# Optimization experiments

Measured on AMD Instinct MI355X. Metric: run time of the kernel, lower is better.

Reference implementation:

```python
import jax, jax.numpy as jnp
import numpy as np
import math

B, N, DIM = 8, 8192, 256
DIM_ATTN, HEAD, RANK = 256, 4, 64
HEAD_DIM = DIM_ATTN // HEAD


def setup_inputs() -> dict:
    key = jax.random.key(0)
    ks = jax.random.split(key, 8)
    x = jax.random.normal(ks[0], (B, N, DIM), dtype=jnp.float32)
    z = jax.random.normal(ks[1], (B, N, DIM), dtype=jnp.float32)
    # nn.Linear(dim, dim_attn): weight (out,in) -> use (in,out) for x @ W
    Wq = jax.random.normal(ks[2], (DIM, DIM_ATTN), dtype=jnp.float32) / np.sqrt(DIM)
    bq = jnp.zeros((DIM_ATTN,), dtype=jnp.float32)
    K = jax.random.normal(ks[3], (RANK, HEAD, HEAD_DIM), dtype=jnp.float32)
    Wv = jax.random.normal(ks[4], (DIM, DIM), dtype=jnp.float32) / np.sqrt(DIM)
    bv = jnp.zeros((DIM,), dtype=jnp.float32)
    alpha = jnp.full((HEAD, 1), math.log(9.0), dtype=jnp.float32)
    beta = jnp.full((HEAD, 1), math.log(0.01), dtype=jnp.float32)
    return {"x": x, "z": z, "Wq": Wq, "bq": bq, "K": K, "Wv": Wv, "bv": bv,
            "alpha": alpha, "beta": beta}


def reference(x, z, Wq, bq, K, Wv, bv, alpha, beta):
    b, n, f = x.shape
    # q: (b, n, head, head_dim)
    q = (z @ Wq + bq).reshape(b, n, HEAD, HEAD_DIM)
    # attn scores over latent rank: (b, n, h, r)
    attn = jnp.einsum('bnhd,rhd->bnhr', q, K) / np.sqrt(HEAD_DIM).astype(np.float32)
    # value projection: (b, n, h, d)
    xv = (x @ Wv + bv).reshape(b, n, HEAD, HEAD_DIM)
    # pool over n with softmax over r: (b, r, h, d)
    pooled = jnp.einsum('bnhr,bnhd->brhd', jax.nn.softmax(attn, axis=-1), xv)
    # redistribute with softmax over n: (b, n, h, d)
    v = jnp.einsum('bnhr,brhd->bnhd', jax.nn.softmax(attn, axis=1), pooled)
    # sigmoid-gated combine; alpha/beta are (head, 1) broadcasting over (h, d)
    out = jax.nn.sigmoid(alpha) * xv + jax.nn.sigmoid(beta) * v
    return out.reshape(b, n, f)
```

## Files before the change

### kernel.cpp

```cpp
#include <hip/hip_runtime.h>
#include <hip/hip_bf16.h>

typedef __hip_bfloat16 bf16;
typedef __attribute__((ext_vector_type(8))) __bf16 bf16x8;
typedef __attribute__((ext_vector_type(4))) float f32x4;

#define BB 8
#define NN 8192
#define DIM 256
#define HEAD 4
#define HD 64
#define RANK 64
#define BN (BB*NN)

__device__ __forceinline__ float b2f(bf16 v){ return __bfloat162float(v); }
__device__ __forceinline__ bf16 f2b(float v){ return __float2bfloat16(v); }
__device__ __forceinline__ unsigned short f2bu(float f){
    bf16 h = __float2bfloat16(f);
    return *(unsigned short*)&h;
}
__device__ __forceinline__ float u2f(unsigned short u){
    unsigned int x = ((unsigned int)u) << 16; return __uint_as_float(x);
}
__device__ __forceinline__ __bf16 f2bb(float f){
    bf16 h = __float2bfloat16(f);
    return *reinterpret_cast<__bf16*>(&h);
}
__device__ __forceinline__ int swz(int k, int outer){
    return (((k >> 3) ^ (outer & 7)) << 3) | (k & 7);
}

__global__ void __launch_bounds__(256) kW(
    const float* __restrict__ Wq, const float* __restrict__ bq,
    const float* __restrict__ Km, const float* __restrict__ Wv,
    unsigned short* __restrict__ WattnT, unsigned short* __restrict__ WvT,
    float* __restrict__ battn)
{
    const int c = blockIdx.x;
    const int h = c >> 6, r = c & 63;
    const int t = threadIdx.x;
    __shared__ float Ks[64];
    if(t < 64) Ks[t] = Km[((size_t)r*HEAD + h)*64 + t];
    __syncthreads();

    const float* wqrow = Wq + (size_t)t*DIM + h*64;
    float a = 0.f;
    #pragma unroll
    for(int d = 0; d < 64; d++) a = fmaf(wqrow[d], Ks[d], a);
    WattnT[(size_t)c*DIM + t] = f2bu(0.125f * a);
    WvT[(size_t)c*DIM + t]    = f2bu(Wv[(size_t)t*DIM + c]);
    if(t == 0){
        float bb = 0.f;
        for(int d = 0; d < 64; d++) bb += bq[h*64+d]*Ks[d];
        battn[c] = 0.125f * bb;
    }
}

__global__ void __launch_bounds__(256) kG(
    const float* __restrict__ x, const float* __restrict__ z,
    const unsigned short* __restrict__ WvT, const unsigned short* __restrict__ WattnT,
    const float* __restrict__ bv, const float* __restrict__ battn,
    float* __restrict__ outF, unsigned short* __restrict__ outB,
    float* __restrict__ Pm, float* __restrict__ Ps)
{
    __shared__ __attribute__((aligned(16))) __bf16 As[2][64][40];

    const int role = blockIdx.x & 1;
    const int tile = blockIdx.x >> 1;

    const float* A            = role ? z : x;
    const unsigned short* WT  = role ? WattnT : WvT;
    const float* bias         = role ? battn : bv;

    const int t    = threadIdx.x;
    const int lane = t & 63;
    const int w    = t >> 6;
    const int q    = lane >> 4;
    const int l15  = lane & 15;
    const int brow = tile * 64;

    f32x4 acc[4][4];
    #pragma unroll
    for(int tm = 0; tm < 4; tm++)
        #pragma unroll
        for(int tn = 0; tn < 4; tn++) acc[tm][tn] = (f32x4){0.f,0.f,0.f,0.f};

    const int arow = t >> 2, aseg = t & 3;
    const float* aSrc = A + (size_t)(brow + arow)*DIM + aseg*8;
    const unsigned short* bBase = WT + (size_t)(w*64 + l15)*DIM + q*8;

    {
        float4 v0 = *(const float4*)(aSrc + 0);
        float4 v1 = *(const float4*)(aSrc + 4);
        __attribute__((aligned(16))) __bf16 tmp[8] = {
            f2bb(v0.x), f2bb(v0.y), f2bb(v0.z), f2bb(v0.w),
            f2bb(v1.x), f2bb(v1.y), f2bb(v1.z), f2bb(v1.w)};
        *(bf16x8*)&As[0][arow][aseg*8] = *(bf16x8*)tmp;
    }
    float4 s0 = *(const float4*)(aSrc + 32);
    float4 s1 = *(const float4*)(aSrc + 36);
    bf16x8 bcur[4];
    #pragma unroll
    for(int tn = 0; tn < 4; tn++)
        bcur[tn] = *(const bf16x8*)(bBase + (size_t)tn*16*DIM);
    __syncthreads();

    #pragma unroll
    for(int step = 0; step < 8; step++){
        const int cur = step & 1;
        const int k0  = step * 32;

        bf16x8 bnext[4];
        if(step < 7){
            #pragma unroll
            for(int tn = 0; tn < 4; tn++)
                bnext[tn] = *(const bf16x8*)(bBase + (size_t)tn*16*DIM + k0 + 32);
        }

        bf16x8 af[4];
        #pragma unroll
        for(int tm = 0; tm < 4; tm++) af[tm] = *(const bf16x8*)&As[cur][tm*16 + l15][q*8];
        #pragma unroll
        for(int tm = 0; tm < 4; tm++)
            #pragma unroll
            for(int tn = 0; tn < 4; tn++)
                acc[tm][tn] = __builtin_amdgcn_mfma_f32_16x16x32_bf16(
                    af[tm], bcur[tn], acc[tm][tn], 0, 0, 0);

        if(step < 7){
            __attribute__((aligned(16))) __bf16 tmp[8] = {
                f2bb(s0.x), f2bb(s0.y), f2bb(s0.z), f2bb(s0.w),
                f2bb(s1.x), f2bb(s1.y), f2bb(s1.z), f2bb(s1.w)};
            *(bf16x8*)&As[cur^1][arow][aseg*8] = *(bf16x8*)tmp;
        }
        if(step < 6){
            s0 = *(const float4*)(aSrc + (step+2)*32 + 0);
            s1 = *(const float4*)(aSrc + (step+2)*32 + 4);
        }
        #pragma unroll
        for(int tn = 0; tn < 4; tn++) bcur[tn] = bnext[tn];
        __syncthreads();
    }

    if(role){
        const int b  = brow >> 13;
        const int nb = brow & 8191;
        const size_t blk = tile;
        #pragma unroll
        for(int tn = 0; tn < 4; tn++){
            int col = w*64 + tn*16 + l15;
            int hh = col >> 6, rr = col & 63;
            float bcol = bias[col];
            float rv[16];
            float m16 = -1e30f;
            #pragma unroll
            for(int tm = 0; tm < 4; tm++){
                #pragma unroll
                for(int reg = 0; reg < 4; reg++){
                    float v = acc[tm][tn][reg] + bcol;
                    unsigned short ub = f2bu(v);
                    int n = nb + tm*16 + q*4 + reg;
                    outB[(((size_t)(b*HEAD + hh))*NN + n)*64 + rr] = ub;
                    float vr = u2f(ub);
                    rv[tm*4+reg] = vr;
                    m16 = fmaxf(m16, vr);
                }
            }
            float s16 = 0.f;
            #pragma unroll
            for(int i = 0; i < 16; i++) s16 += __expf(rv[i] - m16);
            #pragma unroll
            for(int off = 16; off <= 32; off <<= 1){
                float m2 = __shfl_xor(m16, off, 64);
                float s2 = __shfl_xor(s16, off, 64);
                float nm = fmaxf(m16, m2);
                s16 = s16*__expf(m16-nm) + s2*__expf(m2-nm);
                m16 = nm;
            }
            if(q == 0){
                Pm[blk*256 + col] = m16;
                Ps[blk*256 + col] = s16;
            }
        }
    } else {
        #pragma unroll
        for(int tn = 0; tn < 4; tn++){
            int col = w*64 + tn*16 + l15;
            float bcol = bias[col];
            #pragma unroll
            for(int tm = 0; tm < 4; tm++){
                #pragma unroll
                for(int reg = 0; reg < 4; reg++){
                    int grow = brow + tm*16 + q*4 + reg;
                    outF[(size_t)grow*256 + col] = acc[tm][tn][reg] + bcol;
                }
            }
        }
    }
}

__global__ void __launch_bounds__(256) kC(const float* __restrict__ Pm, const float* __restrict__ Ps,
                                          float* __restrict__ M, float* __restrict__ S)
{
    const int b = blockIdx.x, col = threadIdx.x;
    float m = -1e30f;
    for(int c = 0; c < 128; c++)
        m = fmaxf(m, Pm[(size_t)(b*128 + c)*256 + col]);
    float s = 0.f;
    for(int c = 0; c < 128; c++){
        size_t i = (size_t)(b*128 + c)*256 + col;
        s += Ps[i] * __expf(Pm[i] - m);
    }
    M[b*256 + col] = m;
    S[b*256 + col] = s;
}

__global__ void __launch_bounds__(256) kD(const unsigned short* __restrict__ attn,
                                          const float* __restrict__ xv,
                                          float* __restrict__ pooledT)
{
    __shared__ unsigned short s1T[64*256];
    __shared__ unsigned short xvT[64*256];

    const int t = threadIdx.x, lane = t & 63, w = t >> 6;
    const int bh = blockIdx.x, chunk = blockIdx.y;
    const int b = bh >> 2, h = bh & 3;
    const int n0 = chunk * 256;
    const int row = t;

    {
        const uint4* ap = (const uint4*)(attn + ((size_t)bh*NN + n0 + row)*64);
        uint4 ar[8];
        #pragma unroll
        for(int c = 0; c < 8; c++) ar[c] = ap[c];
        float vals[64];
        #pragma unroll
        for(int c = 0; c < 8; c++){
            unsigned int uu[4] = {ar[c].x, ar[c].y, ar[c].z, ar[c].w};
            #pragma unroll
            for(int p = 0; p < 4; p++){
                vals[c*8 + p*2 + 0] = __uint_as_float(uu[p] << 16);
                vals[c*8 + p*2 + 1] = __uint_as_float(uu[p] & 0xffff0000u);
            }
        }
        float mx = -1e30f;
        #pragma unroll
        for(int r = 0; r < 64; r++) mx = fmaxf(mx, vals[r]);
        float s = 0.f;
        #pragma unroll
        for(int r = 0; r < 64; r++){
            float e = __expf(vals[r] - mx);
            s += e;
            s1T[r*256 + swz(row, r)] = f2bu(e);
        }
        float rs = 1.f / s;
        const float4* xp = (const float4*)(xv + ((size_t)(b*NN + n0 + row))*256 + h*64);
        #pragma unroll
        for(int c = 0; c < 16; c++){
            float4 f = xp[c];
            int d0 = c*4;
            xvT[(d0+0)*256 + swz(row, d0+0)] = f2bu(f.x * rs);
            xvT[(d0+1)*256 + swz(row, d0+1)] = f2bu(f.y * rs);
            xvT[(d0+2)*256 + swz(row, d0+2)] = f2bu(f.z * rs);
            xvT[(d0+3)*256 + swz(row, d0+3)] = f2bu(f.w * rs);
        }
    }
    __syncthreads();

    const int q = lane >> 4, l15 = lane & 15;
    const int dm = w*16 + l15;
    f32x4 acc[4];
    #pragma unroll
    for(int tn = 0; tn < 4; tn++) acc[tn] = (f32x4){0.f,0.f,0.f,0.f};

    #pragma unroll
    for(int slab = 0; slab < 8; slab++){
        int c = slab*4 + q;
        bf16x8 a = *(const bf16x8*)&xvT[dm*256 + ((c ^ (dm & 7))<<3)];
        #pragma unroll
        for(int tn = 0; tn < 4; tn++){
            int rn = tn*16 + l15;
            bf16x8 bb = *(const bf16x8*)&s1T[rn*256 + ((c ^ (rn & 7))<<3)];
            acc[tn] = __builtin_amdgcn_mfma_f32_16x16x32_bf16(a, bb, acc[tn], 0, 0, 0);
        }
    }
    #pragma unroll
    for(int tn = 0; tn < 4; tn++){
        #pragma unroll
        for(int reg = 0; reg < 4; reg++){
            int d = w*16 + q*4 + reg;
            int r = tn*16 + l15;
            atomicAdd(&pooledT[((size_t)bh*64 + d)*64 + r], acc[tn][reg]);
        }
    }
}

__global__ void __launch_bounds__(256) kE(const unsigned short* __restrict__ attn,
                                          const float* __restrict__ xvin,
                                          const float* __restrict__ pooledT,
                                          const float* __restrict__ Mst, const float* __restrict__ Sst,
                                          const float* __restrict__ alpha, const float* __restrict__ beta,
                                          float* __restrict__ out)
{
    __shared__ unsigned short s2t[256*64];
    __shared__ unsigned short plT[64*64];
    __shared__ float Ms[64], Sinv[64];

    const int t = threadIdx.x, lane = t & 63, w = t >> 6;
    const int bh = blockIdx.x, chunk = blockIdx.y;
    const int b = bh >> 2, h = bh & 3;
    const int n0 = chunk * 256;
    const int row = t;

    if(t < 64){
        Ms[t]   = Mst[b*256 + h*64 + t];
        Sinv[t] = 1.f / Sst[b*256 + h*64 + t];
    }
    {
        int d = t >> 2, seg = t & 3;
        const float4* pp = (const float4*)(pooledT + ((size_t)bh*64 + d)*64 + seg*16);
        float4 p0 = pp[0], p1 = pp[1], p2 = pp[2], p3 = pp[3];
        __attribute__((aligned(16))) unsigned short tmp[16] = {
            f2bu(p0.x),f2bu(p0.y),f2bu(p0.z),f2bu(p0.w),
            f2bu(p1.x),f2bu(p1.y),f2bu(p1.z),f2bu(p1.w),
            f2bu(p2.x),f2bu(p2.y),f2bu(p2.z),f2bu(p2.w),
            f2bu(p3.x),f2bu(p3.y),f2bu(p3.z),f2bu(p3.w)};
        int c0 = seg*2;
        *(uint4*)&plT[d*64 + (((c0+0) ^ (d&7))<<3)] = *(uint4*)&tmp[0];
        *(uint4*)&plT[d*64 + (((c0+1) ^ (d&7))<<3)] = *(uint4*)&tmp[8];
    }
    __syncthreads();

    {
        const uint4* ap = (const uint4*)(attn + ((size_t)bh*NN + n0 + row)*64);
        #pragma unroll
        for(int c = 0; c < 8; c++){
            uint4 u = ap[c];
            unsigned int uu[4] = {u.x, u.y, u.z, u.w};
            unsigned int ov[4];
            #pragma unroll
            for(int p = 0; p < 4; p++){
                int r = c*8 + p*2;
                float v0 = __uint_as_float(uu[p] << 16);
                float v1 = __uint_as_float(uu[p] & 0xffff0000u);
                float e0 = __expf(v0 - Ms[r])   * Sinv[r];
                float e1 = __expf(v1 - Ms[r+1]) * Sinv[r+1];
                ov[p] = (unsigned int)f2bu(e0) | ((unsigned int)f2bu(e1) << 16);
            }
            uint4 w4; w4.x = ov[0]; w4.y = ov[1]; w4.z = ov[2]; w4.w = ov[3];
            *(uint4*)&s2t[row*64 + ((c ^ (row&7))<<3)] = w4;
        }
    }
    __syncthreads();

    const int q = lane >> 4, l15 = lane & 15;
    f32x4 acc[4][4];
    #pragma unroll
    for(int tm = 0; tm < 4; tm++)
        #pragma unroll
        for(int tn = 0; tn < 4; tn++) acc[tm][tn] = (f32x4){0.f,0.f,0.f,0.f};

    #pragma unroll
    for(int s = 0; s < 2; s++){
        int c = s*4 + q;
        bf16x8 bfr[4], af[4];
        #pragma unroll
        for(int tn = 0; tn < 4; tn++){
            int dn = tn*16 + l15;
            bfr[tn] = *(const bf16x8*)&plT[dn*64 + ((c ^ (dn&7))<<3)];
        }
        #pragma unroll
        for(int tm = 0; tm < 4; tm++){
            int ra = w*64 + tm*16 + l15;
            af[tm] = *(const bf16x8*)&s2t[ra*64 + ((c ^ (ra&7))<<3)];
        }
        #pragma unroll
        for(int tm = 0; tm < 4; tm++)
            #pragma unroll
            for(int tn = 0; tn < 4; tn++)
                acc[tm][tn] = __builtin_amdgcn_mfma_f32_16x16x32_bf16(
                    af[tm], bfr[tn], acc[tm][tn], 0, 0, 0);
    }

    const float sa = 1.f / (1.f + __expf(-alpha[h]));
    const float sb = 1.f / (1.f + __expf(-beta[h]));
    #pragma unroll
    for(int tm = 0; tm < 4; tm++){
        #pragma unroll
        for(int reg = 0; reg < 4; reg++){
            int rowo = w*64 + tm*16 + q*4 + reg;
            size_t gbase = ((size_t)(b*NN + n0 + rowo))*256 + h*64;
            #pragma unroll
            for(int tn = 0; tn < 4; tn++){
                int d = tn*16 + l15;
                out[gbase + d] = sa*xvin[gbase + d] + sb*acc[tm][tn][reg];
            }
        }
    }
}

extern "C" void kernel_launch(void* const* d_in, const int* in_sizes, int n_in,
                              void* d_out, int out_size, void* d_ws, size_t ws_size,
                              hipStream_t stream)
{
    (void)in_sizes; (void)n_in; (void)out_size; (void)ws_size;
    const float* x     = (const float*)d_in[0];
    const float* z     = (const float*)d_in[1];
    const float* Wq    = (const float*)d_in[2];
    const float* bq    = (const float*)d_in[3];
    const float* Km    = (const float*)d_in[4];
    const float* Wv    = (const float*)d_in[5];
    const float* bv    = (const float*)d_in[6];
    const float* alpha = (const float*)d_in[7];
    const float* beta  = (const float*)d_in[8];
    float* out = (float*)d_out;

    float* xv = out;

    char* ws = (char*)d_ws;
    unsigned short* attn  = (unsigned short*)(ws + 0);
    float* pooledT = (float*)(ws + 33554432);
    float* Mst     = (float*)(ws + 34078720);
    float* Sst     = (float*)(ws + 34086912);
    float* Pm      = (float*)(ws + 34095104);
    float* Ps      = (float*)(ws + 35143680);
    unsigned short* WattnT = (unsigned short*)(ws + 36192256);
    unsigned short* WvT    = (unsigned short*)(ws + 36323328);
    float* battn   = (float*)(ws + 36454400);

    (void)hipMemsetAsync(pooledT, 0, 524288, stream);
    kW<<<dim3(256), 256, 0, stream>>>(Wq, bq, Km, Wv, WattnT, WvT, battn);
    kG<<<dim3(2*BN/64), 256, 0, stream>>>(x, z, WvT, WattnT, bv, battn, xv, attn, Pm, Ps);
    kC<<<dim3(8), 256, 0, stream>>>(Pm, Ps, Mst, Sst);
    kD<<<dim3(32, 32), 256, 0, stream>>>(attn, xv, pooledT);
    kE<<<dim3(32, 32), 256, 0, stream>>>(attn, xv, pooledT, Mst, Sst, alpha, beta, out);
}
```

Baseline: 299.0 us.

## Fold memset and stats kernel into neighbors; stage full A tile in LDS

Zeroing of pooledT moves into the weight-prep kernel, and the per-batch softmax-stat reduction (kC) moves into a few kD blocks. This removes one memset and one kernel launch. The GEMM kernel now converts the whole 64x256 A tile into LDS up front with a single barrier, instead of double-buffering with a barrier per k-step, and keeps two B fragments in flight. The cost is 40KB of LDS per block, which can lower occupancy. The stats are also computed serially by only 8 blocks inside kD.

```diff
diff --git a/kernel.cpp b/kernel.cpp
--- a/kernel.cpp
+++ b/kernel.cpp
@@ -34,11 +34,17 @@
     const float* __restrict__ Wq, const float* __restrict__ bq,
     const float* __restrict__ Km, const float* __restrict__ Wv,
     unsigned short* __restrict__ WattnT, unsigned short* __restrict__ WvT,
-    float* __restrict__ battn)
+    float* __restrict__ battn, float* __restrict__ pooledZ)
 {
     const int c = blockIdx.x;
     const int h = c >> 6, r = c & 63;
     const int t = threadIdx.x;
+
+    {
+        int idx = (blockIdx.x*256 + t)*2;
+        *(float2*)&pooledZ[idx] = (float2){0.f, 0.f};
+    }
+
     __shared__ float Ks[64];
     if(t < 64) Ks[t] = Km[((size_t)r*HEAD + h)*64 + t];
     __syncthreads();
@@ -63,7 +69,7 @@
     float* __restrict__ outF, unsigned short* __restrict__ outB,
     float* __restrict__ Pm, float* __restrict__ Ps)
 {
-    __shared__ __attribute__((aligned(16))) __bf16 As[2][64][40];
+    __shared__ __attribute__((aligned(16))) __bf16 As8[8][64][40];
 
     const int role = blockIdx.x & 1;
     const int tile = blockIdx.x >> 1;
@@ -78,68 +84,60 @@
     const int q    = lane >> 4;
     const int l15  = lane & 15;
     const int brow = tile * 64;
-
-    f32x4 acc[4][4];
-    #pragma unroll
-    for(int tm = 0; tm < 4; tm++)
-        #pragma unroll
-        for(int tn = 0; tn < 4; tn++) acc[tm][tn] = (f32x4){0.f,0.f,0.f,0.f};
-
     const int arow = t >> 2, aseg = t & 3;
+
     const float* aSrc = A + (size_t)(brow + arow)*DIM + aseg*8;
     const unsigned short* bBase = WT + (size_t)(w*64 + l15)*DIM + q*8;
 
-    {
-        float4 v0 = *(const float4*)(aSrc + 0);
-        float4 v1 = *(const float4*)(aSrc + 4);
+    bf16x8 b0[4], b1[4];
+    #pragma unroll
+    for(int tn = 0; tn < 4; tn++)
+        b0[tn] = *(const bf16x8*)(bBase + (size_t)tn*16*DIM);
+    #pragma unroll
+    for(int tn = 0; tn < 4; tn++)
+        b1[tn] = *(const bf16x8*)(bBase + (size_t)tn*16*DIM + 32);
+
+    #pragma unroll
+    for(int s = 0; s < 8; s++){
+        float4 v0 = *(const float4*)(aSrc + s*32);
+        float4 v1 = *(const float4*)(aSrc + s*32 + 4);
         __attribute__((aligned(16))) __bf16 tmp[8] = {
             f2bb(v0.x), f2bb(v0.y), f2bb(v0.z), f2bb(v0.w),
             f2bb(v1.x), f2bb(v1.y), f2bb(v1.z), f2bb(v1.w)};
-        *(bf16x8*)&As[0][arow][aseg*8] = *(bf16x8*)tmp;
-    }
-    float4 s0 = *(const float4*)(aSrc + 32);
-    float4 s1 = *(const float4*)(aSrc + 36);
-    bf16x8 bcur[4];
-    #pragma unroll
-    for(int tn = 0; tn < 4; tn++)
-        bcur[tn] = *(const bf16x8*)(bBase + (size_t)tn*16*DIM);
+        *(bf16x8*)&As8[s][arow][aseg*8] = *(bf16x8*)tmp;
+    }
+
+    f32x4 acc[4][4];
+    #pragma unroll
+    for(int tm = 0; tm < 4; tm++)
+        #pragma unroll
+        for(int tn = 0; tn < 4; tn++) acc[tm][tn] = (f32x4){0.f,0.f,0.f,0.f};
+
     __syncthreads();
 
     #pragma unroll
     for(int step = 0; step < 8; step++){
-        const int cur = step & 1;
-        const int k0  = step * 32;
-
-        bf16x8 bnext[4];
-        if(step < 7){
+        bf16x8 b2[4];
+        if(step < 6){
             #pragma unroll
             for(int tn = 0; tn < 4; tn++)
-                bnext[tn] = *(const bf16x8*)(bBase + (size_t)tn*16*DIM + k0 + 32);
+                b2[tn] = *(const bf16x8*)(bBase + (size_t)tn*16*DIM + (step+2)*32);
         }
 
         bf16x8 af[4];
         #pragma unroll
-        for(int tm = 0; tm < 4; tm++) af[tm] = *(const bf16x8*)&As[cur][tm*16 + l15][q*8];
+        for(int tm = 0; tm < 4; tm++)
+            af[tm] = *(const bf16x8*)&As8[step][tm*16 + l15][q*8];
+
         #pragma unroll
         for(int tm = 0; tm < 4; tm++)
             #pragma unroll
             for(int tn = 0; tn < 4; tn++)
                 acc[tm][tn] = __builtin_amdgcn_mfma_f32_16x16x32_bf16(
-                    af[tm], bcur[tn], acc[tm][tn], 0, 0, 0);
-
-        if(step < 7){
-            __attribute__((aligned(16))) __bf16 tmp[8] = {
-                f2bb(s0.x), f2bb(s0.y), f2bb(s0.z), f2bb(s0.w),
-                f2bb(s1.x), f2bb(s1.y), f2bb(s1.z), f2bb(s1.w)};
-            *(bf16x8*)&As[cur^1][arow][aseg*8] = *(bf16x8*)tmp;
-        }
-        if(step < 6){
-            s0 = *(const float4*)(aSrc + (step+2)*32 + 0);
-            s1 = *(const float4*)(aSrc + (step+2)*32 + 4);
-        }
-        #pragma unroll
-        for(int tn = 0; tn < 4; tn++) bcur[tn] = bnext[tn];
-        __syncthreads();
+                    af[tm], b0[tn], acc[tm][tn], 0, 0, 0);
+
+        #pragma unroll
+        for(int tn = 0; tn < 4; tn++){ b0[tn] = b1[tn]; b1[tn] = b2[tn]; }
     }
 
     if(role){
@@ -199,25 +197,11 @@
     }
 }
 
-__global__ void __launch_bounds__(256) kC(const float* __restrict__ Pm, const float* __restrict__ Ps,
-                                          float* __restrict__ M, float* __restrict__ S)
-{
-    const int b = blockIdx.x, col = threadIdx.x;
-    float m = -1e30f;
-    for(int c = 0; c < 128; c++)
-        m = fmaxf(m, Pm[(size_t)(b*128 + c)*256 + col]);
-    float s = 0.f;
-    for(int c = 0; c < 128; c++){
-        size_t i = (size_t)(b*128 + c)*256 + col;
-        s += Ps[i] * __expf(Pm[i] - m);
-    }
-    M[b*256 + col] = m;
-    S[b*256 + col] = s;
-}
-
 __global__ void __launch_bounds__(256) kD(const unsigned short* __restrict__ attn,
                                           const float* __restrict__ xv,
-                                          float* __restrict__ pooledT)
+                                          float* __restrict__ pooledT,
+                                          const float* __restrict__ Pm, const float* __restrict__ Ps,
+                                          float* __restrict__ Mst, float* __restrict__ Sst)
 {
     __shared__ unsigned short s1T[64*256];
     __shared__ unsigned short xvT[64*256];
@@ -227,6 +211,20 @@
     const int b = bh >> 2, h = bh & 3;
     const int n0 = chunk * 256;
     const int row = t;
+
+    if(chunk == 0 && (bh & 3) == 0){
+        const int bb = bh >> 2, col = t;
+        float m = -1e30f;
+        for(int c = 0; c < 128; c++)
+            m = fmaxf(m, Pm[(size_t)(bb*128 + c)*256 + col]);
+        float s = 0.f;
+        for(int c = 0; c < 128; c++){
+            size_t i = (size_t)(bb*128 + c)*256 + col;
+            s += Ps[i] * __expf(Pm[i] - m);
+        }
+        Mst[bb*256 + col] = m;
+        Sst[bb*256 + col] = s;
+    }
 
     {
         const uint4* ap = (const uint4*)(attn + ((size_t)bh*NN + n0 + row)*64);
@@ -428,10 +426,8 @@
     unsigned short* WvT    = (unsigned short*)(ws + 36323328);
     float* battn   = (float*)(ws + 36454400);
 
-    (void)hipMemsetAsync(pooledT, 0, 524288, stream);
-    kW<<<dim3(256), 256, 0, stream>>>(Wq, bq, Km, Wv, WattnT, WvT, battn);
+    kW<<<dim3(256), 256, 0, stream>>>(Wq, bq, Km, Wv, WattnT, WvT, battn, pooledT);
     kG<<<dim3(2*BN/64), 256, 0, stream>>>(x, z, WvT, WattnT, bv, battn, xv, attn, Pm, Ps);
-    kC<<<dim3(8), 256, 0, stream>>>(Pm, Ps, Mst, Sst);
-    kD<<<dim3(32, 32), 256, 0, stream>>>(attn, xv, pooledT);
+    kD<<<dim3(32, 32), 256, 0, stream>>>(attn, xv, pooledT, Pm, Ps, Mst, Sst);
     kE<<<dim3(32, 32), 256, 0, stream>>>(attn, xv, pooledT, Mst, Sst, alpha, beta, out);
 }
```

Result: faster. 289.3 us (-3.2%).
